# Optimization experiments

Hardware: AMD Instinct MI355X
Metric: run time of the kernel (lower is better)

## Reference

```python
import jax, jax.numpy as jnp
import numpy as np

N_LAYERS = 2

def setup_inputs() -> dict:
    key = jax.random.key(0)
    ks = jax.random.split(key, 11)
    B, T, S, H, V = 32, 64, 128, 1024, 32000
    dec_input = jax.random.randint(ks[0], (B, T), 0, V)
    h0 = jax.random.normal(ks[1], (N_LAYERS, B, H), jnp.float32)
    c0 = jax.random.normal(ks[2], (N_LAYERS, B, H), jnp.float32)
    encoder_outputs = jax.random.normal(ks[3], (B, S, H), jnp.float32)
    emb = jax.random.normal(ks[4], (V, H), jnp.float32) * 0.02
    emb = emb.at[0].set(0.0)  # padding_idx = 0
    W_ih = jax.random.normal(ks[5], (N_LAYERS, 4 * H, H), jnp.float32) * 0.02
    W_hh = jax.random.normal(ks[6], (N_LAYERS, 4 * H, H), jnp.float32) * 0.02
    b_ih = jax.random.normal(ks[7], (N_LAYERS, 4 * H), jnp.float32) * 0.02
    b_hh = jax.random.normal(ks[8], (N_LAYERS, 4 * H), jnp.float32) * 0.02
    cls_W = jax.random.normal(ks[9], (V, H), jnp.float32) * 0.02
    cls_b = jax.random.normal(ks[10], (V,), jnp.float32) * 0.02
    return dict(dec_input=dec_input, h0=h0, c0=c0, encoder_outputs=encoder_outputs,
                emb=emb, W_ih=W_ih, W_hh=W_hh, b_ih=b_ih, b_hh=b_hh,
                cls_W=cls_W, cls_b=cls_b)


def reference(dec_input, h0, c0, encoder_outputs, emb, W_ih, W_hh, b_ih, b_hh, cls_W, cls_b):
    # embedding (+dropout p=0) then relu, as in the torch forward
    x = jax.nn.relu(jnp.take(emb, dec_input, axis=0))  # [B,T,H]

    def step(carry, x_t):  # x_t: [B,H]
        h, c = carry  # each [L,B,H]
        inp = x_t
        new_h, new_c = [], []
        for i in range(N_LAYERS):
            gates = inp @ W_ih[i].T + b_ih[i] + h[i] @ W_hh[i].T + b_hh[i]  # [B,4H]
            ig, fg, gg, og = jnp.split(gates, 4, axis=-1)  # PyTorch LSTMCell gate order
            ci = jax.nn.sigmoid(fg) * c[i] + jax.nn.sigmoid(ig) * jnp.tanh(gg)
            hi = jax.nn.sigmoid(og) * jnp.tanh(ci)
            new_h.append(hi)
            new_c.append(ci)
            # residual (dims match since embedding_dim == rnn_dim)
            inp = hi + inp
        last = inp  # StackLSTMCell returns residual-accumulated output
        # dot attention: scores = context bmm target -> softmax (combine Linear output is discarded upstream)
        attn = jax.nn.softmax(jnp.einsum('bsh,bh->bs', encoder_outputs, last), axis=-1)
        return (jnp.stack(new_h), jnp.stack(new_c)), (last, attn)

    (hT, cT), (outs, attns) = jax.lax.scan(step, (h0, c0), jnp.swapaxes(x, 0, 1))
    outputs = jnp.swapaxes(outs, 0, 1)  # [B,T,H]
    logits = jnp.einsum('bth,vh->btv', outputs, cls_W) + cls_b  # [B,T,V]
    attn_scores = jnp.transpose(attns, (1, 2, 0))  # stack dim=2 -> [B,S,T]
    return logits, hT, cT, attn_scores
```

## Files before the change

### kernel.cpp

```cpp
#include <hip/hip_runtime.h>
#include <math.h>

typedef _Float16 f16x8 __attribute__((ext_vector_type(8)));
typedef _Float16 f16x4 __attribute__((ext_vector_type(4)));
typedef float    f32x4 __attribute__((ext_vector_type(4)));
typedef unsigned long long u64;
typedef unsigned int u32;

#define ALOAD(p)    __hip_atomic_load((p), __ATOMIC_RELAXED, __HIP_MEMORY_SCOPE_AGENT)
#define ASTORE(p,v) __hip_atomic_store((p), (v), __ATOMIC_RELAXED, __HIP_MEMORY_SCOPE_AGENT)

__global__ __launch_bounds__(256) void k_prep(
    const float* __restrict__ W_ih, _Float16* __restrict__ Wih_h,
    const int* __restrict__ dec, const float* __restrict__ emb,
    float* __restrict__ xf, _Float16* __restrict__ xh,
    const float* __restrict__ W_hh, _Float16* __restrict__ Pk0, _Float16* __restrict__ Pk1,
    const float* __restrict__ h0, const float* __restrict__ c0,
    float* __restrict__ c, _Float16* __restrict__ h0S, _Float16* __restrict__ h1S,
    int* __restrict__ bar) {
  const int bid = blockIdx.x;
  const int tid = threadIdx.x;
  if (bid < 2048) {
#pragma unroll
    for (int q = 0; q < 4; ++q) {
      int i = q * 524288 + bid * 256 + tid;
      float4 v = ((const float4*)W_ih)[i];
      f16x4 o;
      o.x = (_Float16)v.x; o.y = (_Float16)v.y; o.z = (_Float16)v.z; o.w = (_Float16)v.w;
      ((f16x4*)Wih_h)[i] = o;
    }
  } else if (bid < 4096) {
    int i = (bid - 2048) * 256 + tid;
    int r = i >> 8, c4 = i & 255;
    int b = r & 31, t = r >> 5;
    int tok = dec[b * 64 + t];
    float4 v = ((const float4*)(emb + (size_t)tok * 1024))[c4];
    v.x = fmaxf(v.x, 0.f); v.y = fmaxf(v.y, 0.f); v.z = fmaxf(v.z, 0.f); v.w = fmaxf(v.w, 0.f);
    ((float4*)(xf + (size_t)r * 1024))[c4] = v;
    f16x4 o;
    o.x = (_Float16)v.x; o.y = (_Float16)v.y; o.z = (_Float16)v.z; o.w = (_Float16)v.w;
    ((f16x4*)(xh + (size_t)r * 1024))[c4] = o;
  } else if (bid < 8192) {
    int li = (bid - 4096) * 256 + tid;
    int mat = li >> 19;
    int li2 = li & 524287;
    int row = li2 >> 7, k8l = li2 & 127;
    const float* s = (mat ? (W_hh + (size_t)4096 * 1024) : (W_ih + (size_t)4096 * 1024))
                     + (size_t)row * 1024 + k8l * 8;
    int g = row >> 10, u = row & 1023, jb = u >> 4, col = u & 15;
    int k8g = mat * 128 + k8l;
    int kh = k8g >> 5, rem = k8g & 31, st = rem >> 2, kslot = rem & 3;
    size_t idx = ((size_t)(((jb * 8 + kh) * 8 + st) * 4 + g)) * 64 + kslot * 16 + col;
    f16x8 o;
#pragma unroll
    for (int j = 0; j < 8; ++j) o[j] = (_Float16)s[j];
    *(f16x8*)(Pk1 + idx * 8) = o;
  } else if (bid < 10240) {
    int li = (bid - 8192) * 256 + tid;
    int row = li >> 7, k8 = li & 127;
    const float* s = W_hh + (size_t)row * 1024 + k8 * 8;
    int g = row >> 10, u = row & 1023, jb = u >> 4, col = u & 15;
    int kh = k8 >> 4, rem = k8 & 15, st = rem >> 2, kslot = rem & 3;
    size_t idx = ((size_t)(((jb * 8 + kh) * 4 + st) * 4 + g)) * 64 + kslot * 16 + col;
    f16x8 o;
#pragma unroll
    for (int j = 0; j < 8; ++j) o[j] = (_Float16)s[j];
    *(f16x8*)(Pk0 + idx * 8) = o;
  } else {
    int i = (bid - 10240) * 256 + tid;
    float hv = h0[i];
    c[i] = c0[i];
    if (i < 32768) h0S[i] = (_Float16)hv;
    else           h1S[i - 32768] = (_Float16)hv;
    if (i < 640) bar[i] = 0;
  }
}

__global__ __launch_bounds__(512) void k_gemm0b(const _Float16* __restrict__ A,
                                                const _Float16* __restrict__ Bm,
                                                const float* __restrict__ bias0,
                                                const float* __restrict__ bias1,
                                                float* __restrict__ C) {
  __shared__ _Float16 lds2[32768];
  const int tid = threadIdx.x;
  const int lane = tid & 63;
  const int w = tid >> 6;
  const int wm = w >> 2, wn = w & 3;
  const int r0 = tid & 255, kb0 = tid >> 8;
  const int m = blockIdx.y, nt = blockIdx.x;
  const _Float16* Ab = A + (size_t)m * 256 * 1024;
  const _Float16* Bb = Bm + (size_t)nt * 256 * 1024;
  f16x8 pa0, pa1, pb0, pb1;
  pa0 = *(const f16x8*)(Ab + r0 * 1024 + kb0 * 8);
  pa1 = *(const f16x8*)(Ab + r0 * 1024 + (kb0 + 2) * 8);
  pb0 = *(const f16x8*)(Bb + r0 * 1024 + kb0 * 8);
  pb1 = *(const f16x8*)(Bb + r0 * 1024 + (kb0 + 2) * 8);
  f32x4 acc[8][4] = {};
  for (int kc = 0; kc < 32; ++kc) {
    _Float16* Ac = lds2 + (kc & 1) * 8192;
    _Float16* Bc = lds2 + 16384 + (kc & 1) * 8192;
    *(f16x8*)(Ac + kb0 * 2048 + r0 * 8) = pa0;
    *(f16x8*)(Ac + (kb0 + 2) * 2048 + r0 * 8) = pa1;
    *(f16x8*)(Bc + kb0 * 2048 + r0 * 8) = pb0;
    *(f16x8*)(Bc + (kb0 + 2) * 2048 + r0 * 8) = pb1;
    if (kc + 1 < 32) {
      int ko = (kc + 1) * 32;
      pa0 = *(const f16x8*)(Ab + r0 * 1024 + ko + kb0 * 8);
      pa1 = *(const f16x8*)(Ab + r0 * 1024 + ko + (kb0 + 2) * 8);
      pb0 = *(const f16x8*)(Bb + r0 * 1024 + ko + kb0 * 8);
      pb1 = *(const f16x8*)(Bb + r0 * 1024 + ko + (kb0 + 2) * 8);
    }
    __syncthreads();
    const int kb = lane >> 4;
    f16x8 af[8], bf[4];
#pragma unroll
    for (int mf = 0; mf < 8; ++mf) {
      int row = wm * 128 + mf * 16 + (lane & 15);
      af[mf] = *(const f16x8*)(Ac + kb * 2048 + row * 8);
    }
#pragma unroll
    for (int nf = 0; nf < 4; ++nf) {
      int row = wn * 64 + nf * 16 + (lane & 15);
      bf[nf] = *(const f16x8*)(Bc + kb * 2048 + row * 8);
    }
#pragma unroll
    for (int mf = 0; mf < 8; ++mf)
#pragma unroll
      for (int nf = 0; nf < 4; ++nf)
        acc[mf][nf] = __builtin_amdgcn_mfma_f32_16x16x32_f16(af[mf], bf[nf], acc[mf][nf], 0, 0, 0);
  }
  const int rl = (lane >> 4) * 4;
#pragma unroll
  for (int mf = 0; mf < 8; ++mf) {
#pragma unroll
    for (int nf = 0; nf < 4; ++nf) {
#pragma unroll
      for (int j = 0; j < 4; ++j) {
        int rg = m * 256 + wm * 128 + mf * 16 + rl + j;
        int ng = nt * 256 + wn * 64 + nf * 16 + (lane & 15);
        C[(size_t)rg * 8192 + ng] = acc[mf][nf][j] + bias0[ng] + bias1[ng];
      }
    }
  }
}

__device__ __forceinline__ void gbar(int* bar) {
  __syncthreads();
  if (threadIdx.x == 0) {
    int* gen = bar + 544;
    int g = ALOAD(gen);
    int grp = blockIdx.x >> 3;
    int a = __hip_atomic_fetch_add(bar + grp * 32, 1, __ATOMIC_RELAXED, __HIP_MEMORY_SCOPE_AGENT);
    if (a == 7) {
      ASTORE(bar + grp * 32, 0);
      int r = __hip_atomic_fetch_add(bar + 512, 1, __ATOMIC_RELAXED, __HIP_MEMORY_SCOPE_AGENT);
      if (r == 15) {
        ASTORE(bar + 512, 0);
        ASTORE(gen, g + 1);
      }
    }
    while (ALOAD(gen) == g) __builtin_amdgcn_s_sleep(1);
  }
  __syncthreads();
}

template <int ROLE>
__device__ __forceinline__ void run_phases(
    int jb, const _Float16* __restrict__ Pk,
    const float* __restrict__ gx, const float* __restrict__ x_f,
    float* __restrict__ c_f,
    _Float16* __restrict__ h0S, _Float16* __restrict__ h1S,
    float* __restrict__ ipfA, float* __restrict__ ipfB,
    float* __restrict__ outs_f, _Float16* __restrict__ outs_h,
    float* __restrict__ outHT, float* __restrict__ outCT,
    int* bar, _Float16* As) {
  constexpr int S = ROLE ? 8 : 4;
  constexpr int NHALF = ROLE ? 2 : 1;
  constexpr int RSH = ROLE ? 8 : 7;
  constexpr int K8M = ROLE ? 255 : 127;
  const int u0 = jb * 16;
  const int tid = threadIdx.x;
  const int lane = tid & 63;
  const int kh = tid >> 6;
  const int col = lane & 15;
  const int kslot = lane >> 4;

  float* cst = c_f + ROLE * 32768;
  const float* gxbase = gx + (ROLE ? 4096 : 0);
  const int cb = tid >> 4, cul = tid & 15, cu = u0 + cul;

  const _Float16* pkbase = Pk + ((size_t)(jb * 8 + kh) * S) * 4 * 512 + lane * 8;
  const int a0off = col * 2056 + kh * S * 32 + kslot * 8;
  const int a1off = a0off + 16 * 2056;

  f16x8 wreg[S * 4];
#pragma unroll
  for (int i = 0; i < S * 4; ++i) wreg[i] = *(const f16x8*)(pkbase + i * 512);

  for (int p = 0; p <= 64; ++p) {
    const bool active = (ROLE == 0) ? (p < 64) : (p > 0);
    if (active) {
      const int t = (ROLE == 0) ? p : p - 1;
      const _Float16* h0r = h0S + (size_t)p * 32768;
      _Float16* h0w = h0S + (size_t)(p + 1) * 32768;
      const _Float16* h1r = h1S + (size_t)(p - 1) * 32768;
      _Float16* h1w = h1S + (size_t)p * 32768;
      const float* ipfr; float* ipfw;
      if (p & 1) { ipfr = ipfA; ipfw = ipfB; }
      else       { ipfr = ipfB; ipfw = ipfA; }

      const float* gxr = gxbase + (size_t)(t * 32 + cb) * 8192;
      float pg0 = gxr[cu], pg1 = gxr[1024 + cu], pg2 = gxr[2048 + cu], pg3 = gxr[3072 + cu];
      float pc = cst[cb * 1024 + cu];
      float px = 0.f, pip = 0.f;
      if (ROLE == 0) px = x_f[(size_t)(t * 32 + cb) * 1024 + cu];
      else           pip = ALOAD(ipfr + cb * 1024 + cu);

#pragma unroll
      for (int hf = 0; hf < NHALF; ++hf) {
        f16x8 sreg[8];
#pragma unroll
        for (int i = 0; i < 8; ++i) {
          int fr = (hf * 8 + i) * 512 + tid;
          int row = fr >> RSH, k8 = fr & K8M;
          const _Float16* s;
          if (ROLE == 0) s = h0r + row * 1024 + k8 * 8;
          else           s = (k8 < 128) ? (h0r + row * 1024 + k8 * 8)
                                        : (h1r + row * 1024 + (k8 - 128) * 8);
          sreg[i] = *(const f16x8*)s;
        }
#pragma unroll
        for (int i = 0; i < 8; ++i) {
          int fr = (hf * 8 + i) * 512 + tid;
          int row = fr >> RSH, k8 = fr & K8M;
          *(f16x8*)(As + row * 2056 + k8 * 8) = sreg[i];
        }
      }
      __syncthreads();

      f32x4 acc[2][4] = {};
#pragma unroll
      for (int s2 = 0; s2 < S; ++s2) {
        f16x8 a0 = *(const f16x8*)(As + a0off + s2 * 32);
        f16x8 a1 = *(const f16x8*)(As + a1off + s2 * 32);
        acc[0][0] = __builtin_amdgcn_mfma_f32_16x16x32_f16(a0, wreg[s2 * 4 + 0], acc[0][0], 0, 0, 0);
        acc[1][0] = __builtin_amdgcn_mfma_f32_16x16x32_f16(a1, wreg[s2 * 4 + 0], acc[1][0], 0, 0, 0);
        acc[0][1] = __builtin_amdgcn_mfma_f32_16x16x32_f16(a0, wreg[s2 * 4 + 1], acc[0][1], 0, 0, 0);
        acc[1][1] = __builtin_amdgcn_mfma_f32_16x16x32_f16(a1, wreg[s2 * 4 + 1], acc[1][1], 0, 0, 0);
        acc[0][2] = __builtin_amdgcn_mfma_f32_16x16x32_f16(a0, wreg[s2 * 4 + 2], acc[0][2], 0, 0, 0);
        acc[1][2] = __builtin_amdgcn_mfma_f32_16x16x32_f16(a1, wreg[s2 * 4 + 2], acc[1][2], 0, 0, 0);
        acc[0][3] = __builtin_amdgcn_mfma_f32_16x16x32_f16(a0, wreg[s2 * 4 + 3], acc[0][3], 0, 0, 0);
        acc[1][3] = __builtin_amdgcn_mfma_f32_16x16x32_f16(a1, wreg[s2 * 4 + 3], acc[1][3], 0, 0, 0);
      }
      __syncthreads();

      float (*gs)[32][68] = (float (*)[32][68])(void*)As;
      const int rl = kslot * 4;
      if (kh < 4) {
#pragma unroll
        for (int m = 0; m < 2; ++m)
#pragma unroll
          for (int g = 0; g < 4; ++g)
#pragma unroll
            for (int j = 0; j < 4; ++j)
              gs[kh][m * 16 + rl + j][g * 16 + col] = acc[m][g][j];
      }
      __syncthreads();
      if (kh >= 4) {
#pragma unroll
        for (int m = 0; m < 2; ++m)
#pragma unroll
          for (int g = 0; g < 4; ++g)
#pragma unroll
            for (int j = 0; j < 4; ++j)
              gs[kh - 4][m * 16 + rl + j][g * 16 + col] += acc[m][g][j];
      }
      __syncthreads();

      {
        float ig = pg0, fg = pg1, gg = pg2, og = pg3;
#pragma unroll
        for (int cc = 0; cc < 4; ++cc) {
          ig += gs[cc][cb][cul];
          fg += gs[cc][cb][16 + cul];
          gg += gs[cc][cb][32 + cul];
          og += gs[cc][cb][48 + cul];
        }
        float si = 1.f / (1.f + expf(-ig));
        float sf = 1.f / (1.f + expf(-fg));
        float so = 1.f / (1.f + expf(-og));
        float ci = sf * pc + si * tanhf(gg);
        float hi = so * tanhf(ci);
        cst[cb * 1024 + cu] = ci;
        if (t == 63) {
          outHT[ROLE * 32768 + cb * 1024 + cu] = hi;
          outCT[ROLE * 32768 + cb * 1024 + cu] = ci;
        }
        if (ROLE == 0) {
          float hn = __shfl_down(hi, 1);
          float ipv = hi + px;
          float ipn = __shfl_down(ipv, 1);
          if ((cul & 1) == 0) {
            union { _Float16 h[2]; u32 v; } ph;
            ph.h[0] = (_Float16)hi; ph.h[1] = (_Float16)hn;
            ASTORE((u32*)(h0w + cb * 1024 + cu), ph.v);
            union { float f[2]; u64 v; } pi;
            pi.f[0] = ipv; pi.f[1] = ipn;
            ASTORE((u64*)(ipfw + cb * 1024 + cu), pi.v);
          }
        } else {
          float hn = __shfl_down(hi, 1);
          float ro = hi + pip;
          float rn = __shfl_down(ro, 1);
          if ((cul & 1) == 0) {
            union { _Float16 h[2]; u32 v; } ph;
            ph.h[0] = (_Float16)hi; ph.h[1] = (_Float16)hn;
            ASTORE((u32*)(h1w + cb * 1024 + cu), ph.v);
            union { _Float16 h[2]; u32 v; } po;
            po.h[0] = (_Float16)ro; po.h[1] = (_Float16)rn;
            ASTORE((u32*)(outs_h + (size_t)(t * 32 + cb) * 1024 + cu), po.v);
          }
          outs_f[(size_t)(t * 32 + cb) * 1024 + cu] = ro;
        }
      }
    }
    gbar(bar);
  }
}

__device__ __forceinline__ void conv_clsW(const float* __restrict__ src,
                                          _Float16* __restrict__ dst, int cb) {
  for (int i = cb * 512 + threadIdx.x; i < 4096000; i += 65536) {
    const f32x4* s = (const f32x4*)(src + (size_t)i * 8);
    f32x4 v0 = __builtin_nontemporal_load(s);
    f32x4 v1 = __builtin_nontemporal_load(s + 1);
    union { _Float16 h[8]; u64 q[2]; } o;
    o.h[0] = (_Float16)v0.x; o.h[1] = (_Float16)v0.y;
    o.h[2] = (_Float16)v0.z; o.h[3] = (_Float16)v0.w;
    o.h[4] = (_Float16)v1.x; o.h[5] = (_Float16)v1.y;
    o.h[6] = (_Float16)v1.z; o.h[7] = (_Float16)v1.w;
    u64* d = (u64*)(dst + (size_t)i * 8);
    ASTORE(d, o.q[0]);
    ASTORE(d + 1, o.q[1]);
  }
}

__device__ __forceinline__ void run_consumer(
    const _Float16* __restrict__ outs_h, const _Float16* __restrict__ clsW_h,
    const float* __restrict__ cls_b, float* __restrict__ out, int* bar, _Float16* lds) {
  __shared__ int tau_s;
  const int tid = threadIdx.x;
  const int lane = tid & 63;
  const int w = tid >> 6;
  const int wm = w >> 2, wn = w & 3;
  int* gen = bar + 544;
  int* wcnt = bar + 576;
  const int r0 = tid & 255, kb0 = tid >> 8;

  if (tid == 0) {
    while (ALOAD(bar + 608) < 128) __builtin_amdgcn_s_sleep(16);
  }
  __syncthreads();

  for (;;) {
    if (tid == 0) tau_s = __hip_atomic_fetch_add(wcnt, 1, __ATOMIC_RELAXED, __HIP_MEMORY_SCOPE_AGENT);
    __syncthreads();
    int tau = tau_s;
    if (tau >= 1000) break;
    int m = tau / 125, nt = tau - m * 125;
    if (tid == 0) {
      int need = 8 * m + 9; if (need > 65) need = 65;
      while (ALOAD(gen) < need) __builtin_amdgcn_s_sleep(64);
    }
    __syncthreads();

    const _Float16* Ab = outs_h + (size_t)m * 256 * 1024;
    const _Float16* Bb = clsW_h + (size_t)nt * 256 * 1024;
    f16x8 pa0, pa1, pb0, pb1;
    pa0 = *(const f16x8*)(Ab + r0 * 1024 + kb0 * 8);
    pa1 = *(const f16x8*)(Ab + r0 * 1024 + (kb0 + 2) * 8);
    pb0 = *(const f16x8*)(Bb + r0 * 1024 + kb0 * 8);
    pb1 = *(const f16x8*)(Bb + r0 * 1024 + (kb0 + 2) * 8);
    f32x4 acc[8][4] = {};
    for (int kc = 0; kc < 32; ++kc) {
      _Float16* Ac = lds + (kc & 1) * 8192;
      _Float16* Bc = lds + 16384 + (kc & 1) * 8192;
      *(f16x8*)(Ac + kb0 * 2048 + r0 * 8) = pa0;
      *(f16x8*)(Ac + (kb0 + 2) * 2048 + r0 * 8) = pa1;
      *(f16x8*)(Bc + kb0 * 2048 + r0 * 8) = pb0;
      *(f16x8*)(Bc + (kb0 + 2) * 2048 + r0 * 8) = pb1;
      if (kc + 1 < 32) {
        int ko = (kc + 1) * 32;
        pa0 = *(const f16x8*)(Ab + r0 * 1024 + ko + kb0 * 8);
        pa1 = *(const f16x8*)(Ab + r0 * 1024 + ko + (kb0 + 2) * 8);
        pb0 = *(const f16x8*)(Bb + r0 * 1024 + ko + kb0 * 8);
        pb1 = *(const f16x8*)(Bb + r0 * 1024 + ko + (kb0 + 2) * 8);
      }
      __syncthreads();
      const int kb = lane >> 4;
      f16x8 af[8], bf[4];
#pragma unroll
      for (int mf = 0; mf < 8; ++mf) {
        int row = wm * 128 + mf * 16 + (lane & 15);
        af[mf] = *(const f16x8*)(Ac + kb * 2048 + row * 8);
      }
#pragma unroll
      for (int nf = 0; nf < 4; ++nf) {
        int row = wn * 64 + nf * 16 + (lane & 15);
        bf[nf] = *(const f16x8*)(Bc + kb * 2048 + row * 8);
      }
#pragma unroll
      for (int mf = 0; mf < 8; ++mf)
#pragma unroll
        for (int nf = 0; nf < 4; ++nf)
          acc[mf][nf] = __builtin_amdgcn_mfma_f32_16x16x32_f16(af[mf], bf[nf], acc[mf][nf], 0, 0, 0);
    }
    const int rl = (lane >> 4) * 4;
#pragma unroll
    for (int mf = 0; mf < 8; ++mf) {
#pragma unroll
      for (int nf = 0; nf < 4; ++nf) {
#pragma unroll
        for (int j = 0; j < 4; ++j) {
          int rg = m * 256 + wm * 128 + mf * 16 + rl + j;
          int tt = rg >> 5, b = rg & 31;
          int ng = nt * 256 + wn * 64 + nf * 16 + (lane & 15);
          __builtin_nontemporal_store(acc[mf][nf][j] + cls_b[ng],
                                      &out[(size_t)(b * 64 + tt) * 32000 + ng]);
        }
      }
    }
  }
}

__global__ __launch_bounds__(512, 1) void k_lstm_fused(
    const _Float16* __restrict__ Pk0, const _Float16* __restrict__ Pk1,
    const float* __restrict__ gx, const float* __restrict__ x_f,
    float* __restrict__ c_f,
    _Float16* __restrict__ h0S, _Float16* __restrict__ h1S,
    float* __restrict__ ipfA, float* __restrict__ ipfB,
    float* __restrict__ outs_f, _Float16* __restrict__ outs_h,
    const float* __restrict__ cls_W, _Float16* __restrict__ clsW_h,
    const float* __restrict__ cls_b,
    float* __restrict__ out_logits,
    float* __restrict__ outHT, float* __restrict__ outCT,
    int* bar) {
  __shared__ _Float16 As[32 * 2056];
  const int bid = blockIdx.x;
  if (bid < 64) {
    run_phases<0>(bid & 63, Pk0, gx, x_f, c_f, h0S, h1S,
                  ipfA, ipfB, outs_f, outs_h, outHT, outCT, bar, As);
  } else if (bid < 128) {
    run_phases<1>(bid & 63, Pk1, gx, x_f, c_f, h0S, h1S,
                  ipfA, ipfB, outs_f, outs_h, outHT, outCT, bar, As);
  } else {
    conv_clsW(cls_W, clsW_h, bid - 128);
    __syncthreads();
    if (threadIdx.x == 0)
      __hip_atomic_fetch_add(bar + 608, 1, __ATOMIC_RELAXED, __HIP_MEMORY_SCOPE_AGENT);
  }
  run_consumer(outs_h, clsW_h, cls_b, out_logits, bar, As);
}

__global__ __launch_bounds__(256) void k_attn(const float* __restrict__ outs,
                                              const float* __restrict__ enc,
                                              float* __restrict__ att) {
  __shared__ float o_s[8][1024];
  __shared__ float sc[8][128];
  const int tid = threadIdx.x;
  const int lane = tid & 63;
  const int w = tid >> 6;
  const int b = blockIdx.x >> 3;
  const int t0 = (blockIdx.x & 7) * 8;
#pragma unroll
  for (int ii = 0; ii < 8; ++ii) {
    int idx = tid + ii * 256;
    int tt = idx >> 8, c4 = idx & 255;
    ((float4*)&o_s[tt][0])[c4] =
        *(const float4*)(outs + (size_t)((t0 + tt) * 32 + b) * 1024 + (size_t)c4 * 4);
  }
  __syncthreads();
  for (int si = 0; si < 32; ++si) {
    int s = w * 32 + si;
    float av[8] = {0, 0, 0, 0, 0, 0, 0, 0};
    const float* er = enc + (size_t)(b * 128 + s) * 1024;
#pragma unroll
    for (int i = 0; i < 4; ++i) {
      int k = i * 256 + lane * 4;
      float4 e = *(const float4*)(er + k);
#pragma unroll
      for (int tt = 0; tt < 8; ++tt) {
        float4 o = *(const float4*)&o_s[tt][k];
        av[tt] += e.x * o.x + e.y * o.y + e.z * o.z + e.w * o.w;
      }
    }
#pragma unroll
    for (int tt = 0; tt < 8; ++tt) {
      float v = av[tt];
#pragma unroll
      for (int off = 32; off > 0; off >>= 1) v += __shfl_down(v, off);
      if (lane == 0) sc[tt][s] = v;
    }
  }
  __syncthreads();
#pragma unroll
  for (int pp = 0; pp < 2; ++pp) {
    int tt = w + pp * 4;
    float a = sc[tt][lane], b2 = sc[tt][64 + lane];
    float m = fmaxf(a, b2);
#pragma unroll
    for (int off = 32; off > 0; off >>= 1) m = fmaxf(m, __shfl_xor(m, off));
    float e0 = expf(a - m), e1 = expf(b2 - m);
    float ss = e0 + e1;
#pragma unroll
    for (int off = 32; off > 0; off >>= 1) ss += __shfl_xor(ss, off);
    float r = 1.f / ss;
    att[(size_t)b * 8192 + (size_t)lane * 64 + t0 + tt] = e0 * r;
    att[(size_t)b * 8192 + (size_t)(64 + lane) * 64 + t0 + tt] = e1 * r;
  }
}

extern "C" void kernel_launch(void* const* d_in, const int* in_sizes, int n_in,
                              void* d_out, int out_size, void* d_ws, size_t ws_size,
                              hipStream_t stream) {
  const int*   dec   = (const int*)d_in[0];
  const float* h0    = (const float*)d_in[1];
  const float* c0    = (const float*)d_in[2];
  const float* enc   = (const float*)d_in[3];
  const float* emb   = (const float*)d_in[4];
  const float* W_ih  = (const float*)d_in[5];
  const float* W_hh  = (const float*)d_in[6];
  const float* b_ih  = (const float*)d_in[7];
  const float* b_hh  = (const float*)d_in[8];
  const float* cls_W = (const float*)d_in[9];
  const float* cls_b = (const float*)d_in[10];
  float* out = (float*)d_out;
  char* ws = (char*)d_ws;

  float*    x_f    = (float*)(ws + 0);
  _Float16* Pk0    = (_Float16*)(ws + 8388608);
  _Float16* h0S    = (_Float16*)(ws + 16777216);
  _Float16* h1S    = (_Float16*)(ws + 21037056);
  _Float16* Pk1    = (_Float16*)(ws + 29360128);
  _Float16* clsW_h = (_Float16*)(ws + 46137344);
  _Float16* Wih_h  = (_Float16*)(ws + 54657024);
  _Float16* x_h    = (_Float16*)(ws + 71434240);
  float*    gx     = (float*)(ws + 111673344);
  float*    outs_f = (float*)(ws + 178782208);
  _Float16* outs_h = (_Float16*)(ws + 187170816);
  float*    c_f    = (float*)(ws + 191627264);
  int*      bar    = (int*)(ws + 192151552);
  float*    ipfA   = (float*)(ws + 192155648);
  float*    ipfB   = (float*)(ws + 192286720);

  k_prep<<<10496, 256, 0, stream>>>(W_ih, Wih_h, dec, emb, x_f, x_h,
                                    W_hh, Pk0, Pk1, h0, c0, c_f, h0S, h1S, bar);
  k_gemm0b<<<dim3(32, 8), 512, 0, stream>>>(x_h, Wih_h, b_ih, b_hh, gx);

  k_lstm_fused<<<256, 512, 0, stream>>>(Pk0, Pk1, gx, x_f, c_f,
                                        h0S, h1S, ipfA, ipfB,
                                        outs_f, outs_h, cls_W, clsW_h, cls_b, out,
                                        out + (size_t)65536000, out + (size_t)65601536,
                                        bar);

  k_attn<<<256, 256, 0, stream>>>(outs_f, enc, out + (size_t)65667072);
}
```

Baseline: 666.2 us.

## Replace global barrier with per-step dataflow flags between LSTM layers

Removes the grid-wide generation barrier that locked both LSTM layers to the same phase. Each block now bumps a per-layer, per-timestep counter when it finishes. Layer 0 waits on its own previous step and lets layer 1 trail by up to four steps through a 4-slot ring of inter-layer buffers, while layer 1 waits only on layer-0 step t and its own step t-1. The classifier consumers poll the layer-1 completion flag instead of the global generation counter. This lets the two layers run decoupled, in exchange for more flag polling and relaxed-atomic ordering that must be correct.

```diff
diff --git a/kernel.cpp b/kernel.cpp
--- a/kernel.cpp
+++ b/kernel.cpp
@@ -9,6 +9,8 @@
 
 #define ALOAD(p)    __hip_atomic_load((p), __ATOMIC_RELAXED, __HIP_MEMORY_SCOPE_AGENT)
 #define ASTORE(p,v) __hip_atomic_store((p), (v), __ATOMIC_RELAXED, __HIP_MEMORY_SCOPE_AGENT)
+#define AADD(p,v)   __hip_atomic_fetch_add((p), (v), __ATOMIC_RELAXED, __HIP_MEMORY_SCOPE_AGENT)
+
 
 __global__ __launch_bounds__(256) void k_prep(
     const float* __restrict__ W_ih, _Float16* __restrict__ Wih_h,
@@ -17,7 +19,7 @@
     const float* __restrict__ W_hh, _Float16* __restrict__ Pk0, _Float16* __restrict__ Pk1,
     const float* __restrict__ h0, const float* __restrict__ c0,
     float* __restrict__ c, _Float16* __restrict__ h0S, _Float16* __restrict__ h1S,
-    int* __restrict__ bar) {
+    int* __restrict__ flg) {
   const int bid = blockIdx.x;
   const int tid = threadIdx.x;
   if (bid < 2048) {
@@ -72,7 +74,7 @@
     c[i] = c0[i];
     if (i < 32768) h0S[i] = (_Float16)hv;
     else           h1S[i - 32768] = (_Float16)hv;
-    if (i < 640) bar[i] = 0;
+    if (i < 2080) flg[i] = 0;
   }
 }
 
@@ -144,36 +146,16 @@
   }
 }
 
-__device__ __forceinline__ void gbar(int* bar) {
-  __syncthreads();
-  if (threadIdx.x == 0) {
-    int* gen = bar + 544;
-    int g = ALOAD(gen);
-    int grp = blockIdx.x >> 3;
-    int a = __hip_atomic_fetch_add(bar + grp * 32, 1, __ATOMIC_RELAXED, __HIP_MEMORY_SCOPE_AGENT);
-    if (a == 7) {
-      ASTORE(bar + grp * 32, 0);
-      int r = __hip_atomic_fetch_add(bar + 512, 1, __ATOMIC_RELAXED, __HIP_MEMORY_SCOPE_AGENT);
-      if (r == 15) {
-        ASTORE(bar + 512, 0);
-        ASTORE(gen, g + 1);
-      }
-    }
-    while (ALOAD(gen) == g) __builtin_amdgcn_s_sleep(1);
-  }
-  __syncthreads();
-}
-
 template <int ROLE>
 __device__ __forceinline__ void run_phases(
     int jb, const _Float16* __restrict__ Pk,
     const float* __restrict__ gx, const float* __restrict__ x_f,
     float* __restrict__ c_f,
     _Float16* __restrict__ h0S, _Float16* __restrict__ h1S,
-    float* __restrict__ ipfA, float* __restrict__ ipfB,
+    float* __restrict__ ipfS,
     float* __restrict__ outs_f, _Float16* __restrict__ outs_h,
     float* __restrict__ outHT, float* __restrict__ outCT,
-    int* bar, _Float16* As) {
+    int* flg, _Float16* As) {
   constexpr int S = ROLE ? 8 : 4;
   constexpr int NHALF = ROLE ? 2 : 1;
   constexpr int RSH = ROLE ? 8 : 7;
@@ -197,134 +179,141 @@
 #pragma unroll
   for (int i = 0; i < S * 4; ++i) wreg[i] = *(const f16x8*)(pkbase + i * 512);
 
-  for (int p = 0; p <= 64; ++p) {
-    const bool active = (ROLE == 0) ? (p < 64) : (p > 0);
-    if (active) {
-      const int t = (ROLE == 0) ? p : p - 1;
-      const _Float16* h0r = h0S + (size_t)p * 32768;
-      _Float16* h0w = h0S + (size_t)(p + 1) * 32768;
-      const _Float16* h1r = h1S + (size_t)(p - 1) * 32768;
-      _Float16* h1w = h1S + (size_t)p * 32768;
-      const float* ipfr; float* ipfw;
-      if (p & 1) { ipfr = ipfA; ipfw = ipfB; }
-      else       { ipfr = ipfB; ipfw = ipfA; }
-
-      const float* gxr = gxbase + (size_t)(t * 32 + cb) * 8192;
-      float pg0 = gxr[cu], pg1 = gxr[1024 + cu], pg2 = gxr[2048 + cu], pg3 = gxr[3072 + cu];
-      float pc = cst[cb * 1024 + cu];
-      float px = 0.f, pip = 0.f;
-      if (ROLE == 0) px = x_f[(size_t)(t * 32 + cb) * 1024 + cu];
-      else           pip = ALOAD(ipfr + cb * 1024 + cu);
-
-#pragma unroll
-      for (int hf = 0; hf < NHALF; ++hf) {
-        f16x8 sreg[8];
-#pragma unroll
-        for (int i = 0; i < 8; ++i) {
-          int fr = (hf * 8 + i) * 512 + tid;
-          int row = fr >> RSH, k8 = fr & K8M;
-          const _Float16* s;
-          if (ROLE == 0) s = h0r + row * 1024 + k8 * 8;
-          else           s = (k8 < 128) ? (h0r + row * 1024 + k8 * 8)
-                                        : (h1r + row * 1024 + (k8 - 128) * 8);
-          sreg[i] = *(const f16x8*)s;
+  for (int t = 0; t < 64; ++t) {
+    if (tid == 0) {
+      if (ROLE == 0) {
+        if (t > 0)  while (ALOAD(flg + (t - 1) * 16) < 64) __builtin_amdgcn_s_sleep(1);
+        if (t >= 4) while (ALOAD(flg + 1024 + (t - 4) * 16) < 64) __builtin_amdgcn_s_sleep(1);
+      } else {
+        while (ALOAD(flg + t * 16) < 64) __builtin_amdgcn_s_sleep(1);
+        if (t > 0) while (ALOAD(flg + 1024 + (t - 1) * 16) < 64) __builtin_amdgcn_s_sleep(1);
+      }
+    }
+    __syncthreads();
+
+    const _Float16* h0r = h0S + (size_t)(ROLE == 0 ? t : t + 1) * 32768;
+    _Float16* h0w = h0S + (size_t)(t + 1) * 32768;
+    const _Float16* h1r = h1S + (size_t)t * 32768;
+    _Float16* h1w = h1S + (size_t)(t + 1) * 32768;
+    const float* ipfr = ipfS + (size_t)(t & 3) * 32768;
+    float* ipfw = ipfS + (size_t)(t & 3) * 32768;
+
+    const float* gxr = gxbase + (size_t)(t * 32 + cb) * 8192;
+    float pg0 = gxr[cu], pg1 = gxr[1024 + cu], pg2 = gxr[2048 + cu], pg3 = gxr[3072 + cu];
+    float pc = cst[cb * 1024 + cu];
+    float px = 0.f, pip = 0.f;
+    if (ROLE == 0) px = x_f[(size_t)(t * 32 + cb) * 1024 + cu];
+    else           pip = ALOAD(ipfr + cb * 1024 + cu);
+
+#pragma unroll
+    for (int hf = 0; hf < NHALF; ++hf) {
+      f16x8 sreg[8];
+#pragma unroll
+      for (int i = 0; i < 8; ++i) {
+        int fr = (hf * 8 + i) * 512 + tid;
+        int row = fr >> RSH, k8 = fr & K8M;
+        const _Float16* s;
+        if (ROLE == 0) s = h0r + row * 1024 + k8 * 8;
+        else           s = (k8 < 128) ? (h0r + row * 1024 + k8 * 8)
+                                      : (h1r + row * 1024 + (k8 - 128) * 8);
+        sreg[i] = *(const f16x8*)s;
+      }
+#pragma unroll
+      for (int i = 0; i < 8; ++i) {
+        int fr = (hf * 8 + i) * 512 + tid;
+        int row = fr >> RSH, k8 = fr & K8M;
+        *(f16x8*)(As + row * 2056 + k8 * 8) = sreg[i];
+      }
+    }
+    __syncthreads();
+
+    f32x4 acc[2][4] = {};
+#pragma unroll
+    for (int s2 = 0; s2 < S; ++s2) {
+      f16x8 a0 = *(const f16x8*)(As + a0off + s2 * 32);
+      f16x8 a1 = *(const f16x8*)(As + a1off + s2 * 32);
+      acc[0][0] = __builtin_amdgcn_mfma_f32_16x16x32_f16(a0, wreg[s2 * 4 + 0], acc[0][0], 0, 0, 0);
+      acc[1][0] = __builtin_amdgcn_mfma_f32_16x16x32_f16(a1, wreg[s2 * 4 + 0], acc[1][0], 0, 0, 0);
+      acc[0][1] = __builtin_amdgcn_mfma_f32_16x16x32_f16(a0, wreg[s2 * 4 + 1], acc[0][1], 0, 0, 0);
+      acc[1][1] = __builtin_amdgcn_mfma_f32_16x16x32_f16(a1, wreg[s2 * 4 + 1], acc[1][1], 0, 0, 0);
+      acc[0][2] = __builtin_amdgcn_mfma_f32_16x16x32_f16(a0, wreg[s2 * 4 + 2], acc[0][2], 0, 0, 0);
+      acc[1][2] = __builtin_amdgcn_mfma_f32_16x16x32_f16(a1, wreg[s2 * 4 + 2], acc[1][2], 0, 0, 0);
+      acc[0][3] = __builtin_amdgcn_mfma_f32_16x16x32_f16(a0, wreg[s2 * 4 + 3], acc[0][3], 0, 0, 0);
+      acc[1][3] = __builtin_amdgcn_mfma_f32_16x16x32_f16(a1, wreg[s2 * 4 + 3], acc[1][3], 0, 0, 0);
+    }
+    __syncthreads();
+
+    float (*gs)[32][68] = (float (*)[32][68])(void*)As;
+    const int rl = kslot * 4;
+    if (kh < 4) {
+#pragma unroll
+      for (int m = 0; m < 2; ++m)
+#pragma unroll
+        for (int g = 0; g < 4; ++g)
+#pragma unroll
+          for (int j = 0; j < 4; ++j)
+            gs[kh][m * 16 + rl + j][g * 16 + col] = acc[m][g][j];
+    }
+    __syncthreads();
+    if (kh >= 4) {
+#pragma unroll
+      for (int m = 0; m < 2; ++m)
+#pragma unroll
+        for (int g = 0; g < 4; ++g)
+#pragma unroll
+          for (int j = 0; j < 4; ++j)
+            gs[kh - 4][m * 16 + rl + j][g * 16 + col] += acc[m][g][j];
+    }
+    __syncthreads();
+
+    {
+      float ig = pg0, fg = pg1, gg = pg2, og = pg3;
+#pragma unroll
+      for (int cc = 0; cc < 4; ++cc) {
+        ig += gs[cc][cb][cul];
+        fg += gs[cc][cb][16 + cul];
+        gg += gs[cc][cb][32 + cul];
+        og += gs[cc][cb][48 + cul];
+      }
+      float si = 1.f / (1.f + expf(-ig));
+      float sf = 1.f / (1.f + expf(-fg));
+      float so = 1.f / (1.f + expf(-og));
+      float ci = sf * pc + si * tanhf(gg);
+      float hi = so * tanhf(ci);
+      cst[cb * 1024 + cu] = ci;
+      if (t == 63) {
+        outHT[ROLE * 32768 + cb * 1024 + cu] = hi;
+        outCT[ROLE * 32768 + cb * 1024 + cu] = ci;
+      }
+      if (ROLE == 0) {
+        float hn = __shfl_down(hi, 1);
+        float ipv = hi + px;
+        float ipn = __shfl_down(ipv, 1);
+        if ((cul & 1) == 0) {
+          union { _Float16 h[2]; u32 v; } ph;
+          ph.h[0] = (_Float16)hi; ph.h[1] = (_Float16)hn;
+          ASTORE((u32*)(h0w + cb * 1024 + cu), ph.v);
+          union { float f[2]; u64 v; } pi;
+          pi.f[0] = ipv; pi.f[1] = ipn;
+          ASTORE((u64*)(ipfw + cb * 1024 + cu), pi.v);
         }
-#pragma unroll
-        for (int i = 0; i < 8; ++i) {
-          int fr = (hf * 8 + i) * 512 + tid;
-          int row = fr >> RSH, k8 = fr & K8M;
-          *(f16x8*)(As + row * 2056 + k8 * 8) = sreg[i];
+      } else {
+        float hn = __shfl_down(hi, 1);
+        float ro = hi + pip;
+        float rn = __shfl_down(ro, 1);
+        if ((cul & 1) == 0) {
+          union { _Float16 h[2]; u32 v; } ph;
+          ph.h[0] = (_Float16)hi; ph.h[1] = (_Float16)hn;
+          ASTORE((u32*)(h1w + cb * 1024 + cu), ph.v);
+          union { _Float16 h[2]; u32 v; } po;
+          po.h[0] = (_Float16)ro; po.h[1] = (_Float16)rn;
+          ASTORE((u32*)(outs_h + (size_t)(t * 32 + cb) * 1024 + cu), po.v);
         }
-      }
-      __syncthreads();
-
-      f32x4 acc[2][4] = {};
-#pragma unroll
-      for (int s2 = 0; s2 < S; ++s2) {
-        f16x8 a0 = *(const f16x8*)(As + a0off + s2 * 32);
-        f16x8 a1 = *(const f16x8*)(As + a1off + s2 * 32);
-        acc[0][0] = __builtin_amdgcn_mfma_f32_16x16x32_f16(a0, wreg[s2 * 4 + 0], acc[0][0], 0, 0, 0);
-        acc[1][0] = __builtin_amdgcn_mfma_f32_16x16x32_f16(a1, wreg[s2 * 4 + 0], acc[1][0], 0, 0, 0);
-        acc[0][1] = __builtin_amdgcn_mfma_f32_16x16x32_f16(a0, wreg[s2 * 4 + 1], acc[0][1], 0, 0, 0);
-        acc[1][1] = __builtin_amdgcn_mfma_f32_16x16x32_f16(a1, wreg[s2 * 4 + 1], acc[1][1], 0, 0, 0);
-        acc[0][2] = __builtin_amdgcn_mfma_f32_16x16x32_f16(a0, wreg[s2 * 4 + 2], acc[0][2], 0, 0, 0);
-        acc[1][2] = __builtin_amdgcn_mfma_f32_16x16x32_f16(a1, wreg[s2 * 4 + 2], acc[1][2], 0, 0, 0);
-        acc[0][3] = __builtin_amdgcn_mfma_f32_16x16x32_f16(a0, wreg[s2 * 4 + 3], acc[0][3], 0, 0, 0);
-        acc[1][3] = __builtin_amdgcn_mfma_f32_16x16x32_f16(a1, wreg[s2 * 4 + 3], acc[1][3], 0, 0, 0);
-      }
-      __syncthreads();
-
-      float (*gs)[32][68] = (float (*)[32][68])(void*)As;
-      const int rl = kslot * 4;
-      if (kh < 4) {
-#pragma unroll
-        for (int m = 0; m < 2; ++m)
-#pragma unroll
-          for (int g = 0; g < 4; ++g)
-#pragma unroll
-            for (int j = 0; j < 4; ++j)
-              gs[kh][m * 16 + rl + j][g * 16 + col] = acc[m][g][j];
-      }
-      __syncthreads();
-      if (kh >= 4) {
-#pragma unroll
-        for (int m = 0; m < 2; ++m)
-#pragma unroll
-          for (int g = 0; g < 4; ++g)
-#pragma unroll
-            for (int j = 0; j < 4; ++j)
-              gs[kh - 4][m * 16 + rl + j][g * 16 + col] += acc[m][g][j];
-      }
-      __syncthreads();
-
-      {
-        float ig = pg0, fg = pg1, gg = pg2, og = pg3;
-#pragma unroll
-        for (int cc = 0; cc < 4; ++cc) {
-          ig += gs[cc][cb][cul];
-          fg += gs[cc][cb][16 + cul];
-          gg += gs[cc][cb][32 + cul];
-          og += gs[cc][cb][48 + cul];
-        }
-        float si = 1.f / (1.f + expf(-ig));
-        float sf = 1.f / (1.f + expf(-fg));
-        float so = 1.f / (1.f + expf(-og));
-        float ci = sf * pc + si * tanhf(gg);
-        float hi = so * tanhf(ci);
-        cst[cb * 1024 + cu] = ci;
-        if (t == 63) {
-          outHT[ROLE * 32768 + cb * 1024 + cu] = hi;
-          outCT[ROLE * 32768 + cb * 1024 + cu] = ci;
-        }
-        if (ROLE == 0) {
-          float hn = __shfl_down(hi, 1);
-          float ipv = hi + px;
-          float ipn = __shfl_down(ipv, 1);
-          if ((cul & 1) == 0) {
-            union { _Float16 h[2]; u32 v; } ph;
-            ph.h[0] = (_Float16)hi; ph.h[1] = (_Float16)hn;
-            ASTORE((u32*)(h0w + cb * 1024 + cu), ph.v);
-            union { float f[2]; u64 v; } pi;
-            pi.f[0] = ipv; pi.f[1] = ipn;
-            ASTORE((u64*)(ipfw + cb * 1024 + cu), pi.v);
-          }
-        } else {
-          float hn = __shfl_down(hi, 1);
-          float ro = hi + pip;
-          float rn = __shfl_down(ro, 1);
-          if ((cul & 1) == 0) {
-            union { _Float16 h[2]; u32 v; } ph;
-            ph.h[0] = (_Float16)hi; ph.h[1] = (_Float16)hn;
-            ASTORE((u32*)(h1w + cb * 1024 + cu), ph.v);
-            union { _Float16 h[2]; u32 v; } po;
-            po.h[0] = (_Float16)ro; po.h[1] = (_Float16)rn;
-            ASTORE((u32*)(outs_h + (size_t)(t * 32 + cb) * 1024 + cu), po.v);
-          }
-          outs_f[(size_t)(t * 32 + cb) * 1024 + cu] = ro;
-        }
-      }
-    }
-    gbar(bar);
+        outs_f[(size_t)(t * 32 + cb) * 1024 + cu] = ro;
+      }
+    }
+    __syncthreads();
+    if (tid == 0) AADD(flg + (ROLE ? 1024 : 0) + t * 16, 1);
   }
 }
 
@@ -347,30 +336,29 @@
 
 __device__ __forceinline__ void run_consumer(
     const _Float16* __restrict__ outs_h, const _Float16* __restrict__ clsW_h,
-    const float* __restrict__ cls_b, float* __restrict__ out, int* bar, _Float16* lds) {
+    const float* __restrict__ cls_b, float* __restrict__ out, int* flg, _Float16* lds) {
   __shared__ int tau_s;
   const int tid = threadIdx.x;
   const int lane = tid & 63;
   const int w = tid >> 6;
   const int wm = w >> 2, wn = w & 3;
-  int* gen = bar + 544;
-  int* wcnt = bar + 576;
+  int* wcnt = flg + 2048;
   const int r0 = tid & 255, kb0 = tid >> 8;
 
   if (tid == 0) {
-    while (ALOAD(bar + 608) < 128) __builtin_amdgcn_s_sleep(16);
+    while (ALOAD(flg + 2064) < 128) __builtin_amdgcn_s_sleep(16);
   }
   __syncthreads();
 
   for (;;) {
-    if (tid == 0) tau_s = __hip_atomic_fetch_add(wcnt, 1, __ATOMIC_RELAXED, __HIP_MEMORY_SCOPE_AGENT);
+    if (tid == 0) tau_s = AADD(wcnt, 1);
     __syncthreads();
     int tau = tau_s;
     if (tau >= 1000) break;
     int m = tau / 125, nt = tau - m * 125;
     if (tid == 0) {
-      int need = 8 * m + 9; if (need > 65) need = 65;
-      while (ALOAD(gen) < need) __builtin_amdgcn_s_sleep(64);
+      int mm = 8 * m + 7; if (mm > 63) mm = 63;
+      while (ALOAD(flg + 1024 + mm * 16) < 64) __builtin_amdgcn_s_sleep(64);
     }
     __syncthreads();
 
@@ -438,28 +426,27 @@
     const float* __restrict__ gx, const float* __restrict__ x_f,
     float* __restrict__ c_f,
     _Float16* __restrict__ h0S, _Float16* __restrict__ h1S,
-    float* __restrict__ ipfA, float* __restrict__ ipfB,
+    float* __restrict__ ipfS,
     float* __restrict__ outs_f, _Float16* __restrict__ outs_h,
     const float* __restrict__ cls_W, _Float16* __restrict__ clsW_h,
     const float* __restrict__ cls_b,
     float* __restrict__ out_logits,
     float* __restrict__ outHT, float* __restrict__ outCT,
-    int* bar) {
+    int* flg) {
   __shared__ _Float16 As[32 * 2056];
   const int bid = blockIdx.x;
   if (bid < 64) {
-    run_phases<0>(bid & 63, Pk0, gx, x_f, c_f, h0S, h1S,
-                  ipfA, ipfB, outs_f, outs_h, outHT, outCT, bar, As);
+    run_phases<0>(bid & 63, Pk0, gx, x_f, c_f, h0S, h1S, ipfS,
+                  outs_f, outs_h, outHT, outCT, flg, As);
   } else if (bid < 128) {
-    run_phases<1>(bid & 63, Pk1, gx, x_f, c_f, h0S, h1S,
-                  ipfA, ipfB, outs_f, outs_h, outHT, outCT, bar, As);
+    run_phases<1>(bid & 63, Pk1, gx, x_f, c_f, h0S, h1S, ipfS,
+                  outs_f, outs_h, outHT, outCT, flg, As);
   } else {
     conv_clsW(cls_W, clsW_h, bid - 128);
     __syncthreads();
-    if (threadIdx.x == 0)
-      __hip_atomic_fetch_add(bar + 608, 1, __ATOMIC_RELAXED, __HIP_MEMORY_SCOPE_AGENT);
-  }
-  run_consumer(outs_h, clsW_h, cls_b, out_logits, bar, As);
+    if (threadIdx.x == 0) AADD(flg + 2064, 1);
+  }
+  run_consumer(outs_h, clsW_h, cls_b, out_logits, flg, As);
 }
 
 __global__ __launch_bounds__(256) void k_attn(const float* __restrict__ outs,
@@ -541,6 +528,8 @@
   _Float16* Pk0    = (_Float16*)(ws + 8388608);
   _Float16* h0S    = (_Float16*)(ws + 16777216);
   _Float16* h1S    = (_Float16*)(ws + 21037056);
+  float*    ipfS   = (float*)(ws + 25296896);
+  int*      flg    = (int*)(ws + 25821184);
   _Float16* Pk1    = (_Float16*)(ws + 29360128);
   _Float16* clsW_h = (_Float16*)(ws + 46137344);
   _Float16* Wih_h  = (_Float16*)(ws + 54657024);
@@ -549,19 +538,16 @@
   float*    outs_f = (float*)(ws + 178782208);
   _Float16* outs_h = (_Float16*)(ws + 187170816);
   float*    c_f    = (float*)(ws + 191627264);
-  int*      bar    = (int*)(ws + 192151552);
-  float*    ipfA   = (float*)(ws + 192155648);
-  float*    ipfB   = (float*)(ws + 192286720);
 
   k_prep<<<10496, 256, 0, stream>>>(W_ih, Wih_h, dec, emb, x_f, x_h,
-                                    W_hh, Pk0, Pk1, h0, c0, c_f, h0S, h1S, bar);
+                                    W_hh, Pk0, Pk1, h0, c0, c_f, h0S, h1S, flg);
   k_gemm0b<<<dim3(32, 8), 512, 0, stream>>>(x_h, Wih_h, b_ih, b_hh, gx);
 
   k_lstm_fused<<<256, 512, 0, stream>>>(Pk0, Pk1, gx, x_f, c_f,
-                                        h0S, h1S, ipfA, ipfB,
+                                        h0S, h1S, ipfS,
                                         outs_f, outs_h, cls_W, clsW_h, cls_b, out,
                                         out + (size_t)65536000, out + (size_t)65601536,
-                                        bar);
+                                        flg);
 
   k_attn<<<256, 256, 0, stream>>>(outs_f, enc, out + (size_t)65667072);
 }
```

Result: slower. 817.7 us (+22.7%).
